# Performance work log

Measured on AMD Instinct MI355X. Metric: run time of the kernel, lower is better.

Reference implementation:

```python
import jax, jax.numpy as jnp
import numpy as np
from jax.ops import segment_sum, segment_max

N, E, DS, DZ = 16384, 262144, 384, 128
H, D, PQ, PV = 12, 16, 4, 8
EPS = 1e-8


def _quat_to_rot(q):
    q = q / jnp.linalg.norm(q, axis=-1, keepdims=True)
    w, x, y, z = q[:, 0], q[:, 1], q[:, 2], q[:, 3]
    R = jnp.stack([
        1 - 2 * (y * y + z * z), 2 * (x * y - w * z), 2 * (x * z + w * y),
        2 * (x * y + w * z), 1 - 2 * (x * x + z * z), 2 * (y * z - w * x),
        2 * (x * z - w * y), 2 * (y * z + w * x), 1 - 2 * (x * x + y * y),
    ], axis=-1).reshape(-1, 3, 3)
    return R


def setup_inputs() -> dict:
    key = jax.random.key(0)
    ks = jax.random.split(key, 20)
    s = jax.random.normal(ks[0], (N, DS), jnp.float32)
    z = jax.random.normal(ks[1], (E, DZ), jnp.float32)
    edge_index = jax.random.randint(ks[2], (E, 2), 0, N, jnp.int64)
    # valid rigid frames: rotation from random unit quaternion + translation
    R = _quat_to_rot(jax.random.normal(ks[3], (N, 4), jnp.float32))
    t = jax.random.normal(ks[4], (N, 3), jnp.float32)
    f = jnp.zeros((N, 4, 4), jnp.float32).at[:, :3, :3].set(R)
    f = f.at[:, :3, 3].set(t).at[:, 3, 3].set(1.0)

    def lin(k, dout, din):
        return jax.random.normal(k, (dout, din), jnp.float32) / np.sqrt(din)

    hc, hpqk, hpv = H * D, H * PQ * 3, H * PV * 3
    s_out_dim = H * (D * 2 + PV * 4)
    params = dict(
        Wq=lin(ks[5], hc, DS), bq=jnp.zeros((hc,), jnp.float32),
        Wk=lin(ks[6], hc, DS), bk=jnp.zeros((hc,), jnp.float32),
        Wv=lin(ks[7], hc, DS), bv=jnp.zeros((hc,), jnp.float32),
        Wb=lin(ks[8], H, DZ), bb=jnp.zeros((H,), jnp.float32),
        Wqp=lin(ks[9], hpqk, DS), bqp=jnp.zeros((hpqk,), jnp.float32),
        Wkp=lin(ks[10], hpqk, DS), bkp=jnp.zeros((hpqk,), jnp.float32),
        Wvp=lin(ks[11], hpv, DS), bvp=jnp.zeros((hpv,), jnp.float32),
        head_weights=jnp.full((H,), 0.541324854612918, jnp.float32),
        Wpair=lin(ks[12], hc, DZ), bpair=jnp.zeros((hc,), jnp.float32),
        Wo=lin(ks[13], DS, s_out_dim), bo=jnp.zeros((DS,), jnp.float32),
    )
    return dict(s=s, z=z, f=f, edge_index=edge_index, **params)


def _ipa(s, z, f, edge_index, Wq, bq, Wk, bk, Wv, bv, Wb, bb,
         Wqp, bqp, Wkp, bkp, Wvp, bvp, head_weights, Wpair, bpair, Wo, bo):
    n = s.shape[0]
    R, t = f[:, :3, :3], f[:, :3, 3]
    idx_i, idx_j = edge_index[:, 0], edge_index[:, 1]

    norm_attn = (3.0 * D) ** 0.5          # (1/(3d))**-0.5 as in source
    norm_bias = 3.0 ** 0.5
    norm_pt = -0.5 * (3.0 * (PQ * 9.0 / 2)) ** 0.5

    q = (s @ Wq.T + bq).reshape(n, H, D)
    k = (s @ Wk.T + bk).reshape(n, H, D)
    v = (s @ Wv.T + bv).reshape(n, H, D)

    def to_global(pts):  # [n,H,P,3] local -> global
        return jnp.einsum('nij,nhpj->nhpi', R, pts) + t[:, None, None, :]

    q_pts = to_global((s @ Wqp.T + bqp).reshape(n, H, PQ, 3))
    k_pts = to_global((s @ Wkp.T + bkp).reshape(n, H, PQ, 3))
    v_pts = to_global((s @ Wvp.T + bvp).reshape(n, H, PV, 3))

    # scalar QK term + learned pair bias, per edge [E,H]
    attn = jnp.einsum('ehd,ehd->eh', q[idx_i], k[idx_j]) * norm_attn
    attn = attn + (z @ Wb.T + bb) * norm_bias
    # point-distance term
    diff = q_pts[idx_i] - k_pts[idx_j]            # [E,H,PQ,3]
    pt_att = (diff ** 2).sum((-1, -2))            # [E,H]
    pt_att = pt_att * (jax.nn.softplus(head_weights) * norm_pt)
    attn = attn + pt_att

    # segment softmax over edges grouped by destination node idx_i
    m = segment_max(attn, idx_i, num_segments=n)          # [N,H]
    ex = jnp.exp(attn - m[idx_i])
    denom = segment_sum(ex, idx_i, num_segments=n)
    a = ex / denom[idx_i]                                  # [E,H]

    o = segment_sum(a[:, :, None] * v[idx_j], idx_i, num_segments=n)  # [N,H,D]
    o = o.reshape(n, H * D)

    o_pts_g = segment_sum(a[:, :, None, None] * v_pts[idx_j], idx_i,
                          num_segments=n)                  # [N,H,PV,3]
    o_pts_g = o_pts_g.reshape(n, H * PV, 3)
    # invert_apply: R^T (p - t)
    o_pts = jnp.einsum('nji,npj->npi', R, o_pts_g - t[:, None, :])
    o_pts_norm = jnp.sqrt((o_pts ** 2).sum(-1) + EPS)      # [N,H*PV]
    o_pts_flat = o_pts.reshape(n, H * PV * 3)

    v_pair = (z @ Wpair.T + bpair).reshape(-1, H, D)       # [E,H,D]
    o_pair = segment_sum(a[:, :, None] * v_pair, idx_i, num_segments=n)
    o_pair = o_pair.reshape(n, H * D)

    o_s = jnp.concatenate([o, o_pts_flat, o_pts_norm, o_pair], axis=-1)
    return o_s @ Wo.T + bo


def reference(s, z, f, edge_index, Wq, bq, Wk, bk, Wv, bv, Wb, bb,
              Wqp, bqp, Wkp, bkp, Wvp, bvp, head_weights, Wpair, bpair, Wo, bo):
    s_out = _ipa(s, z, f, edge_index, Wq, bq, Wk, bk, Wv, bv, Wb, bb,
                 Wqp, bqp, Wkp, bkp, Wvp, bvp, head_weights, Wpair, bpair, Wo, bo)
    return (s_out, z)
```

## Files before the change

kernel.cpp:

```cpp
#include <hip/hip_runtime.h>

#define NNODE 16384
#define NEDGE 262144
#define DS    384
#define DZ    128
#define NH    12
#define HD    16
#define HC    192
#define HPQK  144
#define HPV   288
#define NCAT  1152
#define FEAT  2144
#define SOUT  384

typedef _Float16 f16;
typedef _Float16 f16x8 __attribute__((ext_vector_type(8)));
typedef _Float16 f16x4 __attribute__((ext_vector_type(4)));
typedef _Float16 f16x2 __attribute__((ext_vector_type(2)));
typedef float    f32x4v __attribute__((ext_vector_type(4)));

#define AS3(p) ((__attribute__((address_space(3))) void*)(p))
#define AS1(p) ((const __attribute__((address_space(1))) void*)(p))
#define WAVE_LDS_FENCE() asm volatile("s_waitcnt lgkmcnt(0)" ::: "memory")

__global__ void k_prep(const float* __restrict__ Wq, const float* __restrict__ Wk,
                       const float* __restrict__ Wv, const float* __restrict__ Wqp,
                       const float* __restrict__ Wkp, const float* __restrict__ Wvp,
                       const float* __restrict__ bq, const float* __restrict__ bk,
                       const float* __restrict__ bv, const float* __restrict__ bqp,
                       const float* __restrict__ bkp, const float* __restrict__ bvp,
                       const float* __restrict__ Wb, const float* __restrict__ Wo,
                       const float* __restrict__ Wpair, const float* __restrict__ bpair,
                       const float* __restrict__ hw,
                       f16* __restrict__ Wcat, float* __restrict__ bcat,
                       f16* __restrict__ Wb16, f16* __restrict__ M2,
                       float* __restrict__ gamv)
{
    int t = blockIdx.x * 256 + threadIdx.x;
    const int T0 = NCAT * DS;
    const int T1 = T0 + NCAT;
    const int T2 = T1 + 16 * DZ;
    const int T3 = T2 + SOUT * FEAT;
    const int T4 = T3 + NH;
    if (t < T0) {
        int r = t / DS, c = t - r * DS;
        float v;
        if      (r < 192) v = Wq [(r      ) * DS + c];
        else if (r < 384) v = Wk [(r - 192) * DS + c];
        else if (r < 576) v = Wv [(r - 384) * DS + c];
        else if (r < 720) v = Wqp[(r - 576) * DS + c];
        else if (r < 864) v = Wkp[(r - 720) * DS + c];
        else              v = Wvp[(r - 864) * DS + c];
        Wcat[t] = (f16)v;
    } else if (t < T1) {
        int r = t - T0;
        float v;
        if      (r < 192) v = bq [r];
        else if (r < 384) v = bk [r - 192];
        else if (r < 576) v = bv [r - 384];
        else if (r < 720) v = bqp[r - 576];
        else if (r < 864) v = bkp[r - 720];
        else              v = bvp[r - 864];
        bcat[r] = v;
    } else if (t < T2) {
        int q = t - T1;
        Wb16[q] = (q < NH * DZ) ? (f16)Wb[q] : (f16)0.0f;
    } else if (t < T3) {
        int q = t - T2;
        int r = q / FEAT, c = q - r * FEAT;
        float v = 0.f;
        if (c < 576) {
            v = Wo[r * 768 + c];
        } else if (c < 2112) {
            int h = (c - 576) >> 7, cc = (c - 576) & 127;
            float acc = 0.f;
            #pragma unroll
            for (int d = 0; d < 16; ++d)
                acc += Wo[r * 768 + 576 + h * 16 + d] * Wpair[(h * 16 + d) * DZ + cc];
            v = acc;
        } else if (c < 2124) {
            int h = c - 2112;
            float acc = 0.f;
            #pragma unroll
            for (int d = 0; d < 16; ++d)
                acc += Wo[r * 768 + 576 + h * 16 + d] * bpair[h * 16 + d];
            v = acc;
        }
        M2[q] = (f16)v;
    } else if (t < T4) {
        int h = t - T3;
        gamv[h] = -3.67423461f * log1pf(__expf(hw[h]));
    }
}

__global__ void k_convert_s(const float4* __restrict__ s4, f16* __restrict__ s16)
{
    int t = blockIdx.x * 256 + threadIdx.x;
    float4 v = s4[t];
    f16x4 o = { (f16)v.x, (f16)v.y, (f16)v.z, (f16)v.w };
    *(f16x4*)(s16 + 4 * (size_t)t) = o;
}

__global__ void k_convert_z(const float* __restrict__ z, const int* __restrict__ inv,
                            f16* __restrict__ z16s)
{
    int t = blockIdx.x * 256 + threadIdx.x;
    int e = t >> 1, half = t & 1;
    int pos = inv[e];
    const float4* zr = (const float4*)(z + (size_t)e * DZ + half * 64);
    f16* zo = z16s + (size_t)pos * DZ + half * 64;
    #pragma unroll
    for (int c = 0; c < 16; ++c) {
        float4 v = zr[c];
        f16x4 o = { (f16)v.x, (f16)v.y, (f16)v.z, (f16)v.w };
        *(f16x4*)(zo + 4 * c) = o;
    }
}

__global__ __launch_bounds__(256) void k_zbias(const f16* __restrict__ z16s,
                                               const f16* __restrict__ Wb16,
                                               const float* __restrict__ bb,
                                               float* __restrict__ zbias)
{
    const int wv = threadIdx.x >> 6, lane = threadIdx.x & 63;
    const int row0 = (blockIdx.x * 4 + wv) * 64;
    f16x8 bf[4];
    #pragma unroll
    for (int ks = 0; ks < 4; ++ks)
        bf[ks] = *(const f16x8*)(Wb16 + (lane & 15) * DZ + ks * 32 + (lane >> 4) * 8);
    #pragma unroll
    for (int tt = 0; tt < 4; ++tt) {
        int ra = row0 + tt * 16 + (lane & 15);
        f32x4v acc = {};
        #pragma unroll
        for (int ks = 0; ks < 4; ++ks) {
            f16x8 af = *(const f16x8*)(z16s + (size_t)ra * DZ + ks * 32 + (lane >> 4) * 8);
            acc = __builtin_amdgcn_mfma_f32_16x16x32_f16(af, bf[ks], acc, 0, 0, 0);
        }
        int col = lane & 15;
        if (col < NH) {
            #pragma unroll
            for (int r = 0; r < 4; ++r) {
                int row = row0 + tt * 16 + (lane >> 4) * 4 + r;
                zbias[(size_t)row * NH + col] = (acc[r] + bb[col]) * 1.73205081f;
            }
        }
    }
}

__global__ __launch_bounds__(256) void k_gemm(const f16* __restrict__ A, const f16* __restrict__ B,
                                              const float* __restrict__ bias, float* __restrict__ C,
                                              int M, int N, int K)
{
    __shared__ __align__(16) f16 As[128 * 32];
    __shared__ __align__(16) f16 Bs[128 * 32];
    const int tid = threadIdx.x;
    const int wave = tid >> 6, lane = tid & 63;
    const int bm = blockIdx.x, bn = blockIdx.y;
    const int wm = (wave >> 1) * 64, wn = (wave & 1) * 64;
    f32x4v acc[4][4] = {};
    const int srow = wave * 16 + (lane >> 2);
    const int scol = (lane & 3) * 8;
    const f16* gA0 = A + (size_t)(bm * 128 + srow) * K + scol;
    const f16* gA1 = A + (size_t)(bm * 128 + srow + 64) * K + scol;
    const f16* gB0 = B + (size_t)(bn * 128 + srow) * K + scol;
    const f16* gB1 = B + (size_t)(bn * 128 + srow + 64) * K + scol;
    f16* lA0 = As + wave * 512;
    f16* lA1 = As + (wave + 4) * 512;
    f16* lB0 = Bs + wave * 512;
    f16* lB1 = Bs + (wave + 4) * 512;
    const int fr = lane & 15, fc = (lane >> 4) * 8;
    const int nK = K >> 5;
    for (int kk = 0; kk < nK; ++kk) {
        __syncthreads();
        __builtin_amdgcn_global_load_lds(AS1(gA0), AS3(lA0), 16, 0, 0);
        __builtin_amdgcn_global_load_lds(AS1(gA1), AS3(lA1), 16, 0, 0);
        __builtin_amdgcn_global_load_lds(AS1(gB0), AS3(lB0), 16, 0, 0);
        __builtin_amdgcn_global_load_lds(AS1(gB1), AS3(lB1), 16, 0, 0);
        gA0 += 32; gA1 += 32; gB0 += 32; gB1 += 32;
        __syncthreads();
        f16x8 af[4], bf[4];
        #pragma unroll
        for (int mi = 0; mi < 4; ++mi)
            af[mi] = *(const f16x8*)(As + (wm + mi * 16 + fr) * 32 + fc);
        #pragma unroll
        for (int ni = 0; ni < 4; ++ni)
            bf[ni] = *(const f16x8*)(Bs + (wn + ni * 16 + fr) * 32 + fc);
        #pragma unroll
        for (int mi = 0; mi < 4; ++mi)
            #pragma unroll
            for (int ni = 0; ni < 4; ++ni)
                acc[mi][ni] = __builtin_amdgcn_mfma_f32_16x16x32_f16(af[mi], bf[ni], acc[mi][ni], 0, 0, 0);
    }
    const int r0 = bm * 128 + wm + (lane >> 4) * 4;
    const int c0 = bn * 128 + wn + (lane & 15);
    #pragma unroll
    for (int mi = 0; mi < 4; ++mi)
        #pragma unroll
        for (int ni = 0; ni < 4; ++ni) {
            int col = c0 + ni * 16;
            float b = bias[col];
            #pragma unroll
            for (int r = 0; r < 4; ++r) {
                int row = r0 + mi * 16 + r;
                C[(size_t)row * N + col] = acc[mi][ni][r] + b;
            }
        }
}

__global__ __launch_bounds__(256) void k_gemm16(const f16* __restrict__ A, const f16* __restrict__ B,
                                                const float* __restrict__ bias, f16* __restrict__ C,
                                                int M, int N, int K)
{
    __shared__ __align__(16) f16 As[128 * 32];
    __shared__ __align__(16) f16 Bs[128 * 32];
    const int tid = threadIdx.x;
    const int wave = tid >> 6, lane = tid & 63;
    const int bm = blockIdx.x, bn = blockIdx.y;
    const int wm = (wave >> 1) * 64, wn = (wave & 1) * 64;
    f32x4v acc[4][4] = {};
    const int srow = wave * 16 + (lane >> 2);
    const int scol = (lane & 3) * 8;
    const f16* gA0 = A + (size_t)(bm * 128 + srow) * K + scol;
    const f16* gA1 = A + (size_t)(bm * 128 + srow + 64) * K + scol;
    const f16* gB0 = B + (size_t)(bn * 128 + srow) * K + scol;
    const f16* gB1 = B + (size_t)(bn * 128 + srow + 64) * K + scol;
    f16* lA0 = As + wave * 512;
    f16* lA1 = As + (wave + 4) * 512;
    f16* lB0 = Bs + wave * 512;
    f16* lB1 = Bs + (wave + 4) * 512;
    const int fr = lane & 15, fc = (lane >> 4) * 8;
    const int nK = K >> 5;
    for (int kk = 0; kk < nK; ++kk) {
        __syncthreads();
        __builtin_amdgcn_global_load_lds(AS1(gA0), AS3(lA0), 16, 0, 0);
        __builtin_amdgcn_global_load_lds(AS1(gA1), AS3(lA1), 16, 0, 0);
        __builtin_amdgcn_global_load_lds(AS1(gB0), AS3(lB0), 16, 0, 0);
        __builtin_amdgcn_global_load_lds(AS1(gB1), AS3(lB1), 16, 0, 0);
        gA0 += 32; gA1 += 32; gB0 += 32; gB1 += 32;
        __syncthreads();
        f16x8 af[4], bf[4];
        #pragma unroll
        for (int mi = 0; mi < 4; ++mi)
            af[mi] = *(const f16x8*)(As + (wm + mi * 16 + fr) * 32 + fc);
        #pragma unroll
        for (int ni = 0; ni < 4; ++ni)
            bf[ni] = *(const f16x8*)(Bs + (wn + ni * 16 + fr) * 32 + fc);
        #pragma unroll
        for (int mi = 0; mi < 4; ++mi)
            #pragma unroll
            for (int ni = 0; ni < 4; ++ni)
                acc[mi][ni] = __builtin_amdgcn_mfma_f32_16x16x32_f16(af[mi], bf[ni], acc[mi][ni], 0, 0, 0);
    }
    const int r0 = bm * 128 + wm + (lane >> 4) * 4;
    const int c0 = bn * 128 + wn + (lane & 15);
    #pragma unroll
    for (int mi = 0; mi < 4; ++mi)
        #pragma unroll
        for (int ni = 0; ni < 4; ++ni) {
            int col = c0 + ni * 16;
            float b = bias[col];
            #pragma unroll
            for (int r = 0; r < 4; ++r) {
                int row = r0 + mi * 16 + r;
                C[(size_t)row * N + col] = (f16)(acc[mi][ni][r] + b);
            }
        }
}

__global__ __launch_bounds__(64) void k_nodepost(const f16* __restrict__ raw, const float* __restrict__ fmat,
        f16* __restrict__ Q16, f16* __restrict__ K16, f16* __restrict__ V16,
        f16* __restrict__ QP16, f16* __restrict__ KP16, f16* __restrict__ VP16)
{
    int n = blockIdx.x, l = threadIdx.x;
    const f16* r = raw + (size_t)n * NCAT;
    #pragma unroll
    for (int q = 0; q < 3; ++q) {
        int c = q * 64 + l;
        Q16[(size_t)n * HC + c] = r[c];
        K16[(size_t)n * HC + c] = r[HC + c];
        V16[(size_t)n * HC + c] = r[2 * HC + c];
    }
    const float* fp = fmat + (size_t)n * 16;
    float R00 = fp[0], R01 = fp[1], R02 = fp[2],  t0 = fp[3];
    float R10 = fp[4], R11 = fp[5], R12 = fp[6],  t1 = fp[7];
    float R20 = fp[8], R21 = fp[9], R22 = fp[10], t2 = fp[11];
    if (l < 48) {
        const f16* p = r + 576 + 3 * l;
        float x = (float)p[0], y = (float)p[1], zz = (float)p[2];
        QP16[(size_t)n * HPQK + 3 * l + 0] = (f16)(R00 * x + R01 * y + R02 * zz + t0);
        QP16[(size_t)n * HPQK + 3 * l + 1] = (f16)(R10 * x + R11 * y + R12 * zz + t1);
        QP16[(size_t)n * HPQK + 3 * l + 2] = (f16)(R20 * x + R21 * y + R22 * zz + t2);
        const f16* p2 = r + 720 + 3 * l;
        float x2 = (float)p2[0], y2 = (float)p2[1], z2 = (float)p2[2];
        KP16[(size_t)n * HPQK + 3 * l + 0] = (f16)(R00 * x2 + R01 * y2 + R02 * z2 + t0);
        KP16[(size_t)n * HPQK + 3 * l + 1] = (f16)(R10 * x2 + R11 * y2 + R12 * z2 + t1);
        KP16[(size_t)n * HPQK + 3 * l + 2] = (f16)(R20 * x2 + R21 * y2 + R22 * z2 + t2);
    }
    {
        const f16* p = r + 864 + 3 * l;
        float x = (float)p[0], y = (float)p[1], zz = (float)p[2];
        VP16[(size_t)n * HPV + 3 * l + 0] = (f16)(R00 * x + R01 * y + R02 * zz + t0);
        VP16[(size_t)n * HPV + 3 * l + 1] = (f16)(R10 * x + R11 * y + R12 * zz + t1);
        VP16[(size_t)n * HPV + 3 * l + 2] = (f16)(R20 * x + R21 * y + R22 * zz + t2);
    }
    if (l < 32) {
        int tt = 64 + l;
        const f16* p = r + 864 + 3 * tt;
        float x = (float)p[0], y = (float)p[1], zz = (float)p[2];
        VP16[(size_t)n * HPV + 3 * tt + 0] = (f16)(R00 * x + R01 * y + R02 * zz + t0);
        VP16[(size_t)n * HPV + 3 * tt + 1] = (f16)(R10 * x + R11 * y + R12 * zz + t1);
        VP16[(size_t)n * HPV + 3 * tt + 2] = (f16)(R20 * x + R21 * y + R22 * zz + t2);
    }
}

__global__ void k_zero(int* counts, int* cursor) {
    int t = blockIdx.x * 256 + threadIdx.x;
    if (t < NNODE) counts[t] = 0;
    else if (t < 2 * NNODE) cursor[t - NNODE] = 0;
}
__global__ void k_count(const int* __restrict__ ei, int* counts) {
    int e = blockIdx.x * 256 + threadIdx.x;
    if (e < NEDGE) atomicAdd(&counts[ei[2 * e]], 1);
}
__global__ void k_scan(const int* __restrict__ counts, int* __restrict__ rowptr) {
    __shared__ int lds[256];
    int t = threadIdx.x;
    const int per = NNODE / 256;
    int s = 0;
    for (int i = 0; i < per; ++i) s += counts[t * per + i];
    lds[t] = s; __syncthreads();
    for (int off = 1; off < 256; off <<= 1) {
        int v = (t >= off) ? lds[t - off] : 0;
        __syncthreads();
        lds[t] += v;
        __syncthreads();
    }
    int run = (t == 0) ? 0 : lds[t - 1];
    for (int i = 0; i < per; ++i) { rowptr[t * per + i] = run; run += counts[t * per + i]; }
    if (t == 255) rowptr[NNODE] = run;
}
__global__ void k_scatter(const int* __restrict__ ei, const int* __restrict__ rowptr,
                          int* cursor, int* __restrict__ inv, int* __restrict__ jsorted,
                          int* __restrict__ isorted) {
    int e = blockIdx.x * 256 + threadIdx.x;
    if (e < NEDGE) {
        int i = ei[2 * e];
        int pos = rowptr[i] + atomicAdd(&cursor[i], 1);
        inv[e] = pos;
        jsorted[pos] = ei[2 * e + 1];
        isorted[pos] = i;
    }
}

__global__ __launch_bounds__(256) void k_logits2(
    const int* __restrict__ isorted, const int* __restrict__ jsorted,
    const float* __restrict__ zbias,
    const f16* __restrict__ Q16, const f16* __restrict__ K16,
    const f16* __restrict__ QP16, const f16* __restrict__ KP16,
    const float* __restrict__ gamv, float* __restrict__ attn)
{
    const int pos = blockIdx.x * 256 + threadIdx.x;
    const int i = isorted[pos], j = jsorted[pos];
    const f16x8* qr = (const f16x8*)(Q16 + (size_t)i * HC);
    const f16x8* kr = (const f16x8*)(K16 + (size_t)j * HC);
    const f16* qpp = QP16 + (size_t)i * HPQK;
    const f16* kpp = KP16 + (size_t)j * HPQK;
    const float4* zbp = (const float4*)(zbias + (size_t)pos * NH);
    float4 zb0 = zbp[0], zb1 = zbp[1], zb2 = zbp[2];
    float zb[NH] = { zb0.x, zb0.y, zb0.z, zb0.w, zb1.x, zb1.y, zb1.z, zb1.w,
                     zb2.x, zb2.y, zb2.z, zb2.w };
    float out[NH];
    #pragma unroll
    for (int h = 0; h < NH; ++h) {
        f16x8 q0 = qr[2 * h], q1 = qr[2 * h + 1];
        f16x8 k0 = kr[2 * h], k1 = kr[2 * h + 1];
        float d = 0.f;
        #pragma unroll
        for (int u = 0; u < 8; ++u)
            d += (float)q0[u] * (float)k0[u] + (float)q1[u] * (float)k1[u];
        float pt = 0.f;
        #pragma unroll
        for (int c = 0; c < 3; ++c) {
            f16x4 qpc = *(const f16x4*)(qpp + 12 * h + 4 * c);
            f16x4 kpc = *(const f16x4*)(kpp + 12 * h + 4 * c);
            #pragma unroll
            for (int u = 0; u < 4; ++u) {
                float dd = (float)qpc[u] - (float)kpc[u];
                pt += dd * dd;
            }
        }
        out[h] = 6.92820323f * d + zb[h] + gamv[h] * pt;
    }
    float4* ao = (float4*)(attn + (size_t)pos * NH);
    ao[0] = make_float4(out[0], out[1], out[2], out[3]);
    ao[1] = make_float4(out[4], out[5], out[6], out[7]);
    ao[2] = make_float4(out[8], out[9], out[10], out[11]);
}

__global__ __launch_bounds__(256) void k_soft(
    const int* __restrict__ rowptr, const float* __restrict__ attn,
    f16* __restrict__ a16, f16* __restrict__ feat)
{
    const int lane = threadIdx.x & 63, wv = threadIdx.x >> 6;
    const int slot = lane >> 4, el = lane & 15;
    const int n = blockIdx.x * 16 + wv * 4 + slot;
    const int base = rowptr[n], deg = rowptr[n + 1] - base;

    f16* fo = feat + (size_t)n * FEAT;
    fo[2112 + el]      = (f16)((el < NH && deg > 0) ? 1.0f : 0.0f);
    fo[2112 + 16 + el] = (f16)0.0f;

    float lg[NH];
    if (deg <= 16) {
        if (el < deg) {
            const float4* ar = (const float4*)(attn + (size_t)(base + el) * NH);
            float4 a0 = ar[0], a1 = ar[1], a2 = ar[2];
            lg[0]=a0.x; lg[1]=a0.y; lg[2]=a0.z; lg[3]=a0.w;
            lg[4]=a1.x; lg[5]=a1.y; lg[6]=a1.z; lg[7]=a1.w;
            lg[8]=a2.x; lg[9]=a2.y; lg[10]=a2.z; lg[11]=a2.w;
        } else {
            #pragma unroll
            for (int h = 0; h < NH; ++h) lg[h] = -1e30f;
        }
        #pragma unroll
        for (int h = 0; h < NH; ++h) {
            float v = lg[h];
            v = fmaxf(v, __shfl_xor(v, 1));
            v = fmaxf(v, __shfl_xor(v, 2));
            v = fmaxf(v, __shfl_xor(v, 4));
            v = fmaxf(v, __shfl_xor(v, 8));
            float e = __expf(lg[h] - v);
            float ssum = e;
            ssum += __shfl_xor(ssum, 1);
            ssum += __shfl_xor(ssum, 2);
            ssum += __shfl_xor(ssum, 4);
            ssum += __shfl_xor(ssum, 8);
            lg[h] = (ssum > 0.f) ? e / ssum : 0.f;
        }
        if (el < deg) {
            f16x8 o0, o1;
            #pragma unroll
            for (int h = 0; h < 8; ++h) o0[h] = (f16)lg[h];
            #pragma unroll
            for (int h = 8; h < 12; ++h) o1[h - 8] = (f16)lg[h];
            o1[4] = o1[5] = o1[6] = o1[7] = (f16)0.0f;
            f16* ap = a16 + (size_t)(base + el) * 16;
            *(f16x8*)ap = o0;
            *(f16x8*)(ap + 8) = o1;
        }
    } else {
        const int nch = (deg + 15) >> 4;
        float mx[NH];
        #pragma unroll
        for (int h = 0; h < NH; ++h) mx[h] = -1e30f;
        for (int c = 0; c < nch; ++c) {
            int idx = c * 16 + el;
            if (idx < deg) {
                const float4* ar = (const float4*)(attn + (size_t)(base + idx) * NH);
                float4 a0 = ar[0], a1 = ar[1], a2 = ar[2];
                float v[NH] = { a0.x,a0.y,a0.z,a0.w, a1.x,a1.y,a1.z,a1.w, a2.x,a2.y,a2.z,a2.w };
                #pragma unroll
                for (int h = 0; h < NH; ++h) mx[h] = fmaxf(mx[h], v[h]);
            }
        }
        #pragma unroll
        for (int h = 0; h < NH; ++h) {
            float v = mx[h];
            v = fmaxf(v, __shfl_xor(v, 1));
            v = fmaxf(v, __shfl_xor(v, 2));
            v = fmaxf(v, __shfl_xor(v, 4));
            v = fmaxf(v, __shfl_xor(v, 8));
            mx[h] = v;
        }
        float ls[NH] = {};
        for (int c = 0; c < nch; ++c) {
            int idx = c * 16 + el;
            if (idx < deg) {
                const float4* ar = (const float4*)(attn + (size_t)(base + idx) * NH);
                float4 a0 = ar[0], a1 = ar[1], a2 = ar[2];
                float v[NH] = { a0.x,a0.y,a0.z,a0.w, a1.x,a1.y,a1.z,a1.w, a2.x,a2.y,a2.z,a2.w };
                f16x8 o0, o1;
                #pragma unroll
                for (int h = 0; h < NH; ++h) {
                    float e = __expf(v[h] - mx[h]);
                    ls[h] += e;
                    if (h < 8) o0[h] = (f16)e; else o1[h - 8] = (f16)e;
                }
                o1[4] = o1[5] = o1[6] = o1[7] = (f16)0.0f;
                f16* ap = a16 + (size_t)(base + idx) * 16;
                *(f16x8*)ap = o0;
                *(f16x8*)(ap + 8) = o1;
            }
        }
        float il[NH];
        #pragma unroll
        for (int h = 0; h < NH; ++h) {
            float v = ls[h];
            v += __shfl_xor(v, 1);
            v += __shfl_xor(v, 2);
            v += __shfl_xor(v, 4);
            v += __shfl_xor(v, 8);
            il[h] = (v > 0.f) ? 1.0f / v : 0.f;
        }
        for (int c = 0; c < nch; ++c) {
            int idx = c * 16 + el;
            if (idx < deg) {
                f16* ap = a16 + (size_t)(base + idx) * 16;
                f16x8 o0 = *(f16x8*)ap;
                f16x8 o1 = *(f16x8*)(ap + 8);
                #pragma unroll
                for (int h = 0; h < 8; ++h) o0[h] = (f16)((float)o0[h] * il[h]);
                #pragma unroll
                for (int h = 8; h < 12; ++h) o1[h - 8] = (f16)((float)o1[h - 8] * il[h]);
                *(f16x8*)ap = o0;
                *(f16x8*)(ap + 8) = o1;
            }
        }
    }
}

__global__ __launch_bounds__(256) void k_aggu(
    const int* __restrict__ rowptr, const f16* __restrict__ a16,
    const f16* __restrict__ z16s, f16* __restrict__ feat)
{
    __shared__ f16 ash[4][64 * 16];
    const int wv = threadIdx.x >> 6, lane = threadIdx.x & 63;
    const int n = blockIdx.x * 4 + wv;
    const int base = rowptr[n], deg = rowptr[n + 1] - base;
    float u0[NH] = {}, u1[NH] = {};
    const int nch = (deg + 63) >> 6;
    for (int c = 0; c < nch; ++c) {
        int cl = min(64, deg - c * 64);
        if (lane < cl) {
            const f16x8* ap = (const f16x8*)(a16 + (size_t)(base + c * 64 + lane) * 16);
            *(f16x8*)&ash[wv][lane * 16] = ap[0];
            *(f16x8*)&ash[wv][lane * 16 + 8] = ap[1];
        }
        WAVE_LDS_FENCE();
        for (int kk = 0; kk < cl; ++kk) {
            size_t pos = (size_t)(base + c * 64 + kk);
            f16x2 zv = *(const f16x2*)(z16s + pos * DZ + 2 * lane);
            float z0 = (float)zv[0], z1 = (float)zv[1];
            #pragma unroll
            for (int i = 0; i < 6; ++i) {
                f16x2 a2 = *(const f16x2*)&ash[wv][kk * 16 + 2 * i];
                float a0 = (float)a2[0], a1 = (float)a2[1];
                u0[2 * i]     += a0 * z0; u1[2 * i]     += a0 * z1;
                u0[2 * i + 1] += a1 * z0; u1[2 * i + 1] += a1 * z1;
            }
        }
        WAVE_LDS_FENCE();
    }
    f16* fo = feat + (size_t)n * FEAT + 576;
    #pragma unroll
    for (int h = 0; h < NH; ++h) {
        f16x2 o = { (f16)u0[h], (f16)u1[h] };
        *(f16x2*)(fo + h * DZ + 2 * lane) = o;
    }
}

__global__ __launch_bounds__(256) void k_aggv(
    const int* __restrict__ rowptr, const int* __restrict__ jsorted,
    const f16* __restrict__ a16, const f16* __restrict__ V16,
    const f16* __restrict__ VP16, const float* __restrict__ fmat,
    f16* __restrict__ feat)
{
    __shared__ f16 ash[4][64 * 16];
    __shared__ int jsh[4][64];
    __shared__ float psh[2][HPV];
    const int w4 = threadIdx.x >> 6;
    const int lane = threadIdx.x & 63;
    const int slot = w4 >> 1;
    const int role = w4 & 1;
    const int n = blockIdx.x * 2 + slot;
    const int base = rowptr[n], deg = rowptr[n + 1] - base;
    const int nch = (deg + 63) >> 6;

    float o0 = 0, o1 = 0, o2 = 0;
    const int hA = lane >> 4, hB = (64 + lane) >> 4, hC2 = (128 + lane) >> 4;
    float acc[5] = {};
    int hk[5];
    #pragma unroll
    for (int k = 0; k < 5; ++k) hk[k] = (k * 64 + lane) / 24;

    for (int c = 0; c < nch; ++c) {
        int cl = min(64, deg - c * 64);
        if (lane < cl) {
            size_t pos = (size_t)(base + c * 64 + lane);
            const f16x8* ap = (const f16x8*)(a16 + pos * 16);
            *(f16x8*)&ash[w4][lane * 16] = ap[0];
            *(f16x8*)&ash[w4][lane * 16 + 8] = ap[1];
            jsh[w4][lane] = jsorted[pos];
        }
        WAVE_LDS_FENCE();
        if (role == 0) {
            for (int kk = 0; kk < cl; ++kk) {
                int j = jsh[w4][kk];
                const f16* vr = V16 + (size_t)j * HC;
                float aA = (float)ash[w4][kk * 16 + hA];
                float aB = (float)ash[w4][kk * 16 + hB];
                float aC = (float)ash[w4][kk * 16 + hC2];
                o0 += aA * (float)vr[lane];
                o1 += aB * (float)vr[64 + lane];
                o2 += aC * (float)vr[128 + lane];
            }
        } else {
            for (int kk = 0; kk < cl; ++kk) {
                int j = jsh[w4][kk];
                const f16* vp = VP16 + (size_t)j * HPV;
                #pragma unroll
                for (int k = 0; k < 4; ++k)
                    acc[k] += (float)ash[w4][kk * 16 + hk[k]] * (float)vp[k * 64 + lane];
                if (lane < 32)
                    acc[4] += (float)ash[w4][kk * 16 + hk[4]] * (float)vp[256 + lane];
            }
        }
        WAVE_LDS_FENCE();
    }

    f16* fo = feat + (size_t)n * FEAT;
    if (role == 0) {
        fo[lane] = (f16)o0; fo[64 + lane] = (f16)o1; fo[128 + lane] = (f16)o2;
    } else {
        #pragma unroll
        for (int k = 0; k < 4; ++k) psh[slot][k * 64 + lane] = acc[k];
        if (lane < 32) psh[slot][256 + lane] = acc[4];
        WAVE_LDS_FENCE();
        const float* fp = fmat + (size_t)n * 16;
        float R00 = fp[0], R01 = fp[1], R02 = fp[2],  t0 = fp[3];
        float R10 = fp[4], R11 = fp[5], R12 = fp[6],  t1 = fp[7];
        float R20 = fp[8], R21 = fp[9], R22 = fp[10], t2 = fp[11];
        {
            int P = lane;
            float gx = psh[slot][3 * P] - t0, gy = psh[slot][3 * P + 1] - t1, gz = psh[slot][3 * P + 2] - t2;
            float lx = R00 * gx + R10 * gy + R20 * gz;
            float ly = R01 * gx + R11 * gy + R21 * gz;
            float lz = R02 * gx + R12 * gy + R22 * gz;
            fo[192 + 3 * P] = (f16)lx; fo[192 + 3 * P + 1] = (f16)ly; fo[192 + 3 * P + 2] = (f16)lz;
            fo[480 + P] = (f16)sqrtf(lx * lx + ly * ly + lz * lz + 1e-8f);
        }
        if (lane < 32) {
            int P = 64 + lane;
            float gx = psh[slot][3 * P] - t0, gy = psh[slot][3 * P + 1] - t1, gz = psh[slot][3 * P + 2] - t2;
            float lx = R00 * gx + R10 * gy + R20 * gz;
            float ly = R01 * gx + R11 * gy + R21 * gz;
            float lz = R02 * gx + R12 * gy + R22 * gz;
            fo[192 + 3 * P] = (f16)lx; fo[192 + 3 * P + 1] = (f16)ly; fo[192 + 3 * P + 2] = (f16)lz;
            fo[480 + P] = (f16)sqrtf(lx * lx + ly * ly + lz * lz + 1e-8f);
        }
    }
}

extern "C" void kernel_launch(void* const* d_in, const int* in_sizes, int n_in,
                              void* d_out, int out_size, void* d_ws, size_t ws_size,
                              hipStream_t stream)
{
    (void)in_sizes; (void)n_in; (void)out_size; (void)ws_size;
    const float* s     = (const float*)d_in[0];
    const float* z     = (const float*)d_in[1];
    const float* fmat  = (const float*)d_in[2];
    const int*   ei    = (const int*)d_in[3];
    const float* Wq    = (const float*)d_in[4];
    const float* bq    = (const float*)d_in[5];
    const float* Wk    = (const float*)d_in[6];
    const float* bk    = (const float*)d_in[7];
    const float* Wv    = (const float*)d_in[8];
    const float* bv    = (const float*)d_in[9];
    const float* Wb    = (const float*)d_in[10];
    const float* bb    = (const float*)d_in[11];
    const float* Wqp   = (const float*)d_in[12];
    const float* bqp   = (const float*)d_in[13];
    const float* Wkp   = (const float*)d_in[14];
    const float* bkp   = (const float*)d_in[15];
    const float* Wvp   = (const float*)d_in[16];
    const float* bvp   = (const float*)d_in[17];
    const float* hw    = (const float*)d_in[18];
    const float* Wpair = (const float*)d_in[19];
    const float* bpair = (const float*)d_in[20];
    const float* Wo    = (const float*)d_in[21];
    const float* bo    = (const float*)d_in[22];

    char* w = (char*)d_ws;
    auto alloc = [&](size_t bytes) { char* p = w; w += (bytes + 255) & ~(size_t)255; return p; };
    f16*   s16     = (f16*)  alloc((size_t)NNODE * DS * 2);
    f16*   Wcat    = (f16*)  alloc((size_t)NCAT * DS * 2);
    float* bcat    = (float*)alloc((size_t)NCAT * 4);
    f16*   Wb16    = (f16*)  alloc((size_t)16 * DZ * 2);
    f16*   M2      = (f16*)  alloc((size_t)SOUT * FEAT * 2);
    float* gamv    = (float*)alloc((size_t)NH * 4);
    int*   counts  = (int*)  alloc((size_t)NNODE * 4);
    int*   rowptr  = (int*)  alloc((size_t)(NNODE + 1) * 4);
    int*   cursor  = (int*)  alloc((size_t)NNODE * 4);
    int*   inv     = (int*)  alloc((size_t)NEDGE * 4);
    int*   jsorted = (int*)  alloc((size_t)NEDGE * 4);
    int*   isorted = (int*)  alloc((size_t)NEDGE * 4);
    float* attn    = (float*)alloc((size_t)NEDGE * NH * 4);
    char*  U       = w;
    f16*   raw16   = (f16*)U;
    f16*   feat    = (f16*)U;

    float* zout = (float*)d_out + (size_t)NNODE * DS;
    char*  zr   = (char*)zout;
    f16*   z16s  = (f16*)zr;   zr += (size_t)NEDGE * DZ * 2;
    float* zbias = (float*)zr; zr += (size_t)NEDGE * NH * 4;
    f16*   Q16   = (f16*)zr;   zr += (size_t)NNODE * HC * 2;
    f16*   K16   = (f16*)zr;   zr += (size_t)NNODE * HC * 2;
    f16*   QP16  = (f16*)zr;   zr += (size_t)NNODE * HPQK * 2;
    f16*   KP16  = (f16*)zr;   zr += (size_t)NNODE * HPQK * 2;
    f16*   V16   = (f16*)zr;   zr += (size_t)NNODE * HC * 2;
    f16*   VP16  = (f16*)zr;   zr += (size_t)NNODE * HPV * 2;
    f16*   a16   = (f16*)zr;

    const int PREP_T = NCAT * DS + NCAT + 16 * DZ + SOUT * FEAT + NH;
    k_prep<<<(PREP_T + 255) / 256, 256, 0, stream>>>(Wq, Wk, Wv, Wqp, Wkp, Wvp,
        bq, bk, bv, bqp, bkp, bvp, Wb, Wo, Wpair, bpair, hw, Wcat, bcat, Wb16, M2, gamv);
    k_zero<<<(2 * NNODE) / 256, 256, 0, stream>>>(counts, cursor);
    k_count<<<NEDGE / 256, 256, 0, stream>>>(ei, counts);
    k_scan<<<1, 256, 0, stream>>>(counts, rowptr);
    k_scatter<<<NEDGE / 256, 256, 0, stream>>>(ei, rowptr, cursor, inv, jsorted, isorted);
    k_convert_s<<<(NNODE * DS / 4) / 256, 256, 0, stream>>>((const float4*)s, s16);
    k_convert_z<<<(NEDGE * 2) / 256, 256, 0, stream>>>(z, inv, z16s);
    k_zbias<<<NEDGE / 256, 256, 0, stream>>>(z16s, Wb16, bb, zbias);
    k_gemm16<<<dim3(NNODE / 128, NCAT / 128), 256, 0, stream>>>(s16, Wcat, bcat, raw16,
        NNODE, NCAT, DS);
    k_nodepost<<<NNODE, 64, 0, stream>>>(raw16, fmat, Q16, K16, V16, QP16, KP16, VP16);
    k_logits2<<<NEDGE / 256, 256, 0, stream>>>(isorted, jsorted, zbias, Q16, K16,
        QP16, KP16, gamv, attn);
    k_soft<<<NNODE / 16, 256, 0, stream>>>(rowptr, attn, a16, feat);
    k_aggu<<<NNODE / 4, 256, 0, stream>>>(rowptr, a16, z16s, feat);
    k_aggv<<<NNODE / 2, 256, 0, stream>>>(rowptr, jsorted, a16, V16, VP16, fmat, feat);
    hipMemcpyAsync(zout, z, (size_t)NEDGE * DZ * 4, hipMemcpyDeviceToDevice, stream);
    k_gemm<<<dim3(NNODE / 128, SOUT / 128), 256, 0, stream>>>(feat, M2, bo, (float*)d_out,
        NNODE, SOUT, FEAT);
}
```

Before: 431.4 us.

## Fuse z conversion, pair-bias projection and z passthrough copy into one kernel

Merges the fp16 conversion of z, the MFMA pair-bias kernel and the trailing device-to-device memcpy of z into the output into a single pass. Each thread reads its half-row of z once, writes it to the output, writes the fp16 permuted copy, and computes the 12-head bias in fp32 scalar FMAs, reducing across the pair of threads with a shuffle. Intermediate buffers move from the z-output region into the workspace, since that region is now written early. This removes one full read of z, one read of z16s and two launches, at the cost of scalar FMAs and per-thread weight loads in place of MFMA.

```diff
diff --git a/kernel.cpp b/kernel.cpp
--- a/kernel.cpp
+++ b/kernel.cpp
@@ -29,19 +29,17 @@
                        const float* __restrict__ bq, const float* __restrict__ bk,
                        const float* __restrict__ bv, const float* __restrict__ bqp,
                        const float* __restrict__ bkp, const float* __restrict__ bvp,
-                       const float* __restrict__ Wb, const float* __restrict__ Wo,
+                       const float* __restrict__ Wo,
                        const float* __restrict__ Wpair, const float* __restrict__ bpair,
                        const float* __restrict__ hw,
                        f16* __restrict__ Wcat, float* __restrict__ bcat,
-                       f16* __restrict__ Wb16, f16* __restrict__ M2,
-                       float* __restrict__ gamv)
+                       f16* __restrict__ M2, float* __restrict__ gamv)
 {
     int t = blockIdx.x * 256 + threadIdx.x;
     const int T0 = NCAT * DS;
     const int T1 = T0 + NCAT;
-    const int T2 = T1 + 16 * DZ;
-    const int T3 = T2 + SOUT * FEAT;
-    const int T4 = T3 + NH;
+    const int T2 = T1 + SOUT * FEAT;
+    const int T3 = T2 + NH;
     if (t < T0) {
         int r = t / DS, c = t - r * DS;
         float v;
@@ -64,9 +62,6 @@
         bcat[r] = v;
     } else if (t < T2) {
         int q = t - T1;
-        Wb16[q] = (q < NH * DZ) ? (f16)Wb[q] : (f16)0.0f;
-    } else if (t < T3) {
-        int q = t - T2;
         int r = q / FEAT, c = q - r * FEAT;
         float v = 0.f;
         if (c < 576) {
@@ -87,8 +82,8 @@
             v = acc;
         }
         M2[q] = (f16)v;
-    } else if (t < T4) {
-        int h = t - T3;
+    } else if (t < T3) {
+        int h = t - T2;
         gamv[h] = -3.67423461f * log1pf(__expf(hw[h]));
     }
 }
@@ -101,50 +96,41 @@
     *(f16x4*)(s16 + 4 * (size_t)t) = o;
 }
 
-__global__ void k_convert_z(const float* __restrict__ z, const int* __restrict__ inv,
-                            f16* __restrict__ z16s)
+__global__ __launch_bounds__(256) void k_zfuse(
+    const float* __restrict__ z, const float* __restrict__ Wb,
+    const float* __restrict__ bb, const int* __restrict__ inv,
+    f16* __restrict__ z16s, float* __restrict__ zout, float* __restrict__ zbias)
 {
     int t = blockIdx.x * 256 + threadIdx.x;
     int e = t >> 1, half = t & 1;
     int pos = inv[e];
     const float4* zr = (const float4*)(z + (size_t)e * DZ + half * 64);
-    f16* zo = z16s + (size_t)pos * DZ + half * 64;
+    float4*       zo = (float4*)(zout + (size_t)e * DZ + half * 64);
+    f16*        z16o = z16s + (size_t)pos * DZ + half * 64;
+    const float* wbb = Wb + half * 64;
+    float acc[NH] = {};
     #pragma unroll
     for (int c = 0; c < 16; ++c) {
         float4 v = zr[c];
+        zo[c] = v;
         f16x4 o = { (f16)v.x, (f16)v.y, (f16)v.z, (f16)v.w };
-        *(f16x4*)(zo + 4 * c) = o;
-    }
-}
-
-__global__ __launch_bounds__(256) void k_zbias(const f16* __restrict__ z16s,
-                                               const f16* __restrict__ Wb16,
-                                               const float* __restrict__ bb,
-                                               float* __restrict__ zbias)
-{
-    const int wv = threadIdx.x >> 6, lane = threadIdx.x & 63;
-    const int row0 = (blockIdx.x * 4 + wv) * 64;
-    f16x8 bf[4];
+        *(f16x4*)(z16o + 4 * c) = o;
+        #pragma unroll
+        for (int h = 0; h < NH; ++h) {
+            float4 wv = *(const float4*)(wbb + h * DZ + 4 * c);
+            acc[h] += v.x * wv.x + v.y * wv.y + v.z * wv.z + v.w * wv.w;
+        }
+    }
     #pragma unroll
-    for (int ks = 0; ks < 4; ++ks)
-        bf[ks] = *(const f16x8*)(Wb16 + (lane & 15) * DZ + ks * 32 + (lane >> 4) * 8);
-    #pragma unroll
-    for (int tt = 0; tt < 4; ++tt) {
-        int ra = row0 + tt * 16 + (lane & 15);
-        f32x4v acc = {};
-        #pragma unroll
-        for (int ks = 0; ks < 4; ++ks) {
-            f16x8 af = *(const f16x8*)(z16s + (size_t)ra * DZ + ks * 32 + (lane >> 4) * 8);
-            acc = __builtin_amdgcn_mfma_f32_16x16x32_f16(af, bf[ks], acc, 0, 0, 0);
-        }
-        int col = lane & 15;
-        if (col < NH) {
-            #pragma unroll
-            for (int r = 0; r < 4; ++r) {
-                int row = row0 + tt * 16 + (lane >> 4) * 4 + r;
-                zbias[(size_t)row * NH + col] = (acc[r] + bb[col]) * 1.73205081f;
-            }
-        }
+    for (int h = 0; h < NH; ++h) acc[h] += __shfl_xor(acc[h], 1);
+    if (half == 0) {
+        float4* zb = (float4*)(zbias + (size_t)pos * NH);
+        zb[0] = make_float4((acc[0] + bb[0]) * 1.73205081f, (acc[1] + bb[1]) * 1.73205081f,
+                            (acc[2] + bb[2]) * 1.73205081f, (acc[3] + bb[3]) * 1.73205081f);
+        zb[1] = make_float4((acc[4] + bb[4]) * 1.73205081f, (acc[5] + bb[5]) * 1.73205081f,
+                            (acc[6] + bb[6]) * 1.73205081f, (acc[7] + bb[7]) * 1.73205081f);
+        zb[2] = make_float4((acc[8] + bb[8]) * 1.73205081f, (acc[9] + bb[9]) * 1.73205081f,
+                            (acc[10] + bb[10]) * 1.73205081f, (acc[11] + bb[11]) * 1.73205081f);
     }
 }
 
@@ -686,7 +672,6 @@
     f16*   s16     = (f16*)  alloc((size_t)NNODE * DS * 2);
     f16*   Wcat    = (f16*)  alloc((size_t)NCAT * DS * 2);
     float* bcat    = (float*)alloc((size_t)NCAT * 4);
-    f16*   Wb16    = (f16*)  alloc((size_t)16 * DZ * 2);
     f16*   M2      = (f16*)  alloc((size_t)SOUT * FEAT * 2);
     float* gamv    = (float*)alloc((size_t)NH * 4);
     int*   counts  = (int*)  alloc((size_t)NNODE * 4);
@@ -696,32 +681,30 @@
     int*   jsorted = (int*)  alloc((size_t)NEDGE * 4);
     int*   isorted = (int*)  alloc((size_t)NEDGE * 4);
     float* attn    = (float*)alloc((size_t)NEDGE * NH * 4);
+    f16*   z16s    = (f16*)  alloc((size_t)NEDGE * DZ * 2);
+    float* zbias   = (float*)alloc((size_t)NEDGE * NH * 4);
+    f16*   Q16     = (f16*)  alloc((size_t)NNODE * HC * 2);
+    f16*   K16     = (f16*)  alloc((size_t)NNODE * HC * 2);
+    f16*   QP16    = (f16*)  alloc((size_t)NNODE * HPQK * 2);
+    f16*   KP16    = (f16*)  alloc((size_t)NNODE * HPQK * 2);
+    f16*   V16     = (f16*)  alloc((size_t)NNODE * HC * 2);
+    f16*   VP16    = (f16*)  alloc((size_t)NNODE * HPV * 2);
+    f16*   a16     = (f16*)  alloc((size_t)NEDGE * 16 * 2);
     char*  U       = w;
     f16*   raw16   = (f16*)U;
     f16*   feat    = (f16*)U;
 
     float* zout = (float*)d_out + (size_t)NNODE * DS;
-    char*  zr   = (char*)zout;
-    f16*   z16s  = (f16*)zr;   zr += (size_t)NEDGE * DZ * 2;
-    float* zbias = (float*)zr; zr += (size_t)NEDGE * NH * 4;
-    f16*   Q16   = (f16*)zr;   zr += (size_t)NNODE * HC * 2;
-    f16*   K16   = (f16*)zr;   zr += (size_t)NNODE * HC * 2;
-    f16*   QP16  = (f16*)zr;   zr += (size_t)NNODE * HPQK * 2;
-    f16*   KP16  = (f16*)zr;   zr += (size_t)NNODE * HPQK * 2;
-    f16*   V16   = (f16*)zr;   zr += (size_t)NNODE * HC * 2;
-    f16*   VP16  = (f16*)zr;   zr += (size_t)NNODE * HPV * 2;
-    f16*   a16   = (f16*)zr;
-
-    const int PREP_T = NCAT * DS + NCAT + 16 * DZ + SOUT * FEAT + NH;
+
+    const int PREP_T = NCAT * DS + NCAT + SOUT * FEAT + NH;
     k_prep<<<(PREP_T + 255) / 256, 256, 0, stream>>>(Wq, Wk, Wv, Wqp, Wkp, Wvp,
-        bq, bk, bv, bqp, bkp, bvp, Wb, Wo, Wpair, bpair, hw, Wcat, bcat, Wb16, M2, gamv);
+        bq, bk, bv, bqp, bkp, bvp, Wo, Wpair, bpair, hw, Wcat, bcat, M2, gamv);
     k_zero<<<(2 * NNODE) / 256, 256, 0, stream>>>(counts, cursor);
     k_count<<<NEDGE / 256, 256, 0, stream>>>(ei, counts);
     k_scan<<<1, 256, 0, stream>>>(counts, rowptr);
     k_scatter<<<NEDGE / 256, 256, 0, stream>>>(ei, rowptr, cursor, inv, jsorted, isorted);
     k_convert_s<<<(NNODE * DS / 4) / 256, 256, 0, stream>>>((const float4*)s, s16);
-    k_convert_z<<<(NEDGE * 2) / 256, 256, 0, stream>>>(z, inv, z16s);
-    k_zbias<<<NEDGE / 256, 256, 0, stream>>>(z16s, Wb16, bb, zbias);
+    k_zfuse<<<(NEDGE * 2) / 256, 256, 0, stream>>>(z, Wb, bb, inv, z16s, zout, zbias);
     k_gemm16<<<dim3(NNODE / 128, NCAT / 128), 256, 0, stream>>>(s16, Wcat, bcat, raw16,
         NNODE, NCAT, DS);
     k_nodepost<<<NNODE, 64, 0, stream>>>(raw16, fmat, Q16, K16, V16, QP16, KP16, VP16);
@@ -730,7 +713,6 @@
     k_soft<<<NNODE / 16, 256, 0, stream>>>(rowptr, attn, a16, feat);
     k_aggu<<<NNODE / 4, 256, 0, stream>>>(rowptr, a16, z16s, feat);
     k_aggv<<<NNODE / 2, 256, 0, stream>>>(rowptr, jsorted, a16, V16, VP16, fmat, feat);
-    hipMemcpyAsync(zout, z, (size_t)NEDGE * DZ * 4, hipMemcpyDeviceToDevice, stream);
     k_gemm<<<dim3(NNODE / 128, SOUT / 128), 256, 0, stream>>>(feat, M2, bo, (float*)d_out,
         NNODE, SOUT, FEAT);
 }
```

After: 537.6 us. 1.25x slower.
